# Kernel optimization log

Measured on AMD Instinct MI355X. Metric: run time of the kernel, lower is better.

Reference implementation:

```python
import jax, jax.numpy as jnp
import numpy as np

DISTANCE_WEIGHT = 1.001  # self.distence_weight in the torch module


def setup_inputs() -> dict:
    key = jax.random.key(0)
    k1, k2 = jax.random.split(key)
    B, DIM_IN, DIM_OUT = 1024, 512, 512
    x = jax.random.normal(k1, (B, DIM_IN), dtype=jnp.float32)
    centers = jax.random.normal(k2, (DIM_OUT, DIM_IN), dtype=jnp.float32)
    beta = jnp.ones((DIM_OUT,), dtype=jnp.float32)
    return {"x": x, "centers": centers, "beta": beta}


def reference(x, centers, beta):
    # L1 pairwise distance: [B, dim_out]
    sim = jnp.sum(jnp.abs(x[:, None, :] - centers[None, :, :]), axis=-1)
    # negate, shift by global max * distance_weight, scale by beta
    sim = -sim + jnp.max(sim) * DISTANCE_WEIGHT
    return beta * sim
```

## Files before the change

### kernel.cpp

```cpp
#include <hip/hip_runtime.h>


typedef _Float16 h2 __attribute__((ext_vector_type(2)));
typedef float f4 __attribute__((ext_vector_type(4)));
typedef unsigned int u32x4 __attribute__((ext_vector_type(4)));

#define DIM_K 512
#define DIM_O 512
#define NSPLIT 4
#define KW (DIM_K / NSPLIT)
#define PSTRIDE (1024 * 512)
#define W_DIST 1.001f

__device__ __forceinline__ h2 as_h2(unsigned int u){ h2 r; __builtin_memcpy(&r,&u,4); return r; }
__device__ __forceinline__ unsigned int cvt2(float a, float b){
    auto h = __builtin_amdgcn_cvt_pkrtz(a, b);
    unsigned int r; __builtin_memcpy(&r, &h, 4); return r;
}

__global__ __launch_bounds__(256) void k_sim(const float* __restrict__ X,
                                             const float* __restrict__ C,
                                             float* __restrict__ P)
{
    __shared__ __align__(16) unsigned int xs[64 * 64];
    __shared__ __align__(16) unsigned int cs[64 * 64];
    const int tid = threadIdx.x;
    const int b = blockIdx.x;
    const int ks = b & 3;
    const int ct = (b >> 2) & 7;
    const int rt = b >> 5;
    const int row0 = rt * 64, col0 = ct * 64, kb = ks * KW;

#pragma unroll
    for (int p = 0; p < 4; ++p) {
        const int s = tid + 256 * p;
        const int row = s >> 4, gI = s & 15, gg = gI ^ (row & 7);
        const float* xg = X + (row0 + row) * DIM_K + kb + gg * 8;
        f4 a = *(const f4*)xg; f4 bb = *(const f4*)(xg + 4);
        u32x4 w; w[0]=cvt2(a.x,a.y); w[1]=cvt2(a.z,a.w); w[2]=cvt2(bb.x,bb.y); w[3]=cvt2(bb.z,bb.w);
        *(u32x4*)&xs[row * 64 + gI * 4] = w;
        const float* cg = C + (col0 + row) * DIM_K + kb + gg * 8;
        a = *(const f4*)cg; bb = *(const f4*)(cg + 4);
        u32x4 v; v[0]=cvt2(a.x,a.y); v[1]=cvt2(a.z,a.w); v[2]=cvt2(bb.x,bb.y); v[3]=cvt2(bb.z,bb.w);
        *(u32x4*)&cs[row * 64 + gI * 4] = v;
    }
    __syncthreads();

    const int rb = (tid >> 4) * 4;
    const int tc = tid & 15;
    float acc[4][4] = {};
    const h2 one2 = {(_Float16)1.f, (_Float16)1.f};

#pragma unroll
    for (int g = 0; g < 16; ++g) {
        u32x4 xr[4], cr[4];
#pragma unroll
        for (int i = 0; i < 4; ++i) {
            const int r = rb + i;
            xr[i] = *(const u32x4*)&xs[r * 64 + (g ^ (r & 7)) * 4];
        }
#pragma unroll
        for (int j = 0; j < 4; ++j) {
            const int c = tc + 16 * j;
            cr[j] = *(const u32x4*)&cs[c * 64 + (g ^ (c & 7)) * 4];
        }
#pragma unroll
        for (int k2 = 0; k2 < 4; ++k2) {
#pragma unroll
            for (int i = 0; i < 4; ++i) {
                const h2 a = as_h2(xr[i][k2]);
#pragma unroll
                for (int j = 0; j < 4; ++j) {
                    h2 d = a - as_h2(cr[j][k2]);
                    unsigned int du; __builtin_memcpy(&du, &d, 4);
                    h2 ad = as_h2(du & 0x7fff7fffu);
                    acc[i][j] = __builtin_amdgcn_fdot2(ad, one2, acc[i][j], false);
                }
            }
        }
    }

    float* Pk = P + ks * PSTRIDE;
#pragma unroll
    for (int i = 0; i < 4; ++i) {
        const int row = row0 + rb + i;
#pragma unroll
        for (int j = 0; j < 4; ++j)
            Pk[row * DIM_O + col0 + tc + 16 * j] = acc[i][j];
    }
}

__global__ __launch_bounds__(256) void k_red(const float* __restrict__ P,
                                             float* __restrict__ S,
                                             float* __restrict__ bmax)
{
    const int tid = threadIdx.x;
    const int f = blockIdx.x * 256 + tid;
    const f4* P4 = (const f4*)P;
    const int q = PSTRIDE / 4;
    f4 s = P4[f] + P4[f + q] + P4[f + 2 * q] + P4[f + 3 * q];
    ((f4*)S)[f] = s;
    float m = fmaxf(fmaxf(s.x, s.y), fmaxf(s.z, s.w));
#pragma unroll
    for (int off = 32; off > 0; off >>= 1)
        m = fmaxf(m, __shfl_xor(m, off, 64));
    __shared__ float wm[4];
    if ((tid & 63) == 0) wm[tid >> 6] = m;
    __syncthreads();
    if (tid == 0)
        bmax[blockIdx.x] = fmaxf(fmaxf(wm[0], wm[1]), fmaxf(wm[2], wm[3]));
}

__global__ __launch_bounds__(256) void k_out(float* __restrict__ S,
                                             const float* __restrict__ beta,
                                             const float* __restrict__ bmax)
{
    const int tid = threadIdx.x;
    const int lane = tid & 63;
    float m = 0.f;
#pragma unroll
    for (int i = 0; i < 8; ++i)
        m = fmaxf(m, bmax[lane + 64 * i]);
#pragma unroll
    for (int off = 32; off > 0; off >>= 1)
        m = fmaxf(m, __shfl_xor(m, off, 64));
    const float shift = m * W_DIST;

    const int f = blockIdx.x * 256 + tid;
    f4 s = ((const f4*)S)[f];
    f4 b = ((const f4*)beta)[f & 127];
    f4 r;
    r.x = b.x * (shift - s.x);
    r.y = b.y * (shift - s.y);
    r.z = b.z * (shift - s.z);
    r.w = b.w * (shift - s.w);
    ((f4*)S)[f] = r;
}

extern "C" void kernel_launch(void* const* d_in, const int* in_sizes, int n_in,
                              void* d_out, int out_size, void* d_ws, size_t ws_size,
                              hipStream_t stream) {
    const float* X = (const float*)d_in[0];
    const float* C = (const float*)d_in[1];
    const float* beta = (const float*)d_in[2];
    float* S = (float*)d_out;
    float* P = (float*)d_ws;
    float* bmax = (float*)d_ws + NSPLIT * PSTRIDE;
    k_sim<<<512, 256, 0, stream>>>(X, C, P);
    k_red<<<512, 256, 0, stream>>>(P, S, bmax);
    k_out<<<512, 256, 0, stream>>>(S, beta, bmax);
}
```

Baseline: 79.62 us.

## Split K eight ways with padded LDS rows and occupancy hint

Doubles the K split from four to eight, launching 1024 blocks that each cover 64 K-elements. The XOR-swizzled shared layout is replaced by rows padded to 36 words, and each thread now loads a full 16-float chunk. A minimum-occupancy hint of 4 blocks per CU is added to launch bounds. The aim is more blocks in flight to fill the GPU and hide load latency, but the partial-sum buffer doubles in size, so the reduction kernel reads twice as much data.

Measured after the change: 83.53 us. 1.05x slower.

```diff
diff --git a/kernel.cpp b/kernel.cpp
--- a/kernel.cpp
+++ b/kernel.cpp
@@ -7,8 +7,9 @@
 
 #define DIM_K 512
 #define DIM_O 512
-#define NSPLIT 4
+#define NSPLIT 8
 #define KW (DIM_K / NSPLIT)
+#define LROW 36
 #define PSTRIDE (1024 * 512)
 #define W_DIST 1.001f
 
@@ -18,31 +19,36 @@
     unsigned int r; __builtin_memcpy(&r, &h, 4); return r;
 }
 
-__global__ __launch_bounds__(256) void k_sim(const float* __restrict__ X,
-                                             const float* __restrict__ C,
-                                             float* __restrict__ P)
+__global__ __launch_bounds__(256, 4) void k_sim(const float* __restrict__ X,
+                                                const float* __restrict__ C,
+                                                float* __restrict__ P)
 {
-    __shared__ __align__(16) unsigned int xs[64 * 64];
-    __shared__ __align__(16) unsigned int cs[64 * 64];
+    __shared__ __align__(16) unsigned int xs[64 * LROW];
+    __shared__ __align__(16) unsigned int cs[64 * LROW];
     const int tid = threadIdx.x;
     const int b = blockIdx.x;
-    const int ks = b & 3;
-    const int ct = (b >> 2) & 7;
-    const int rt = b >> 5;
+    const int ks = b & 7;
+    const int ct = (b >> 3) & 7;
+    const int rt = b >> 6;
     const int row0 = rt * 64, col0 = ct * 64, kb = ks * KW;
 
-#pragma unroll
-    for (int p = 0; p < 4; ++p) {
-        const int s = tid + 256 * p;
-        const int row = s >> 4, gI = s & 15, gg = gI ^ (row & 7);
-        const float* xg = X + (row0 + row) * DIM_K + kb + gg * 8;
-        f4 a = *(const f4*)xg; f4 bb = *(const f4*)(xg + 4);
-        u32x4 w; w[0]=cvt2(a.x,a.y); w[1]=cvt2(a.z,a.w); w[2]=cvt2(bb.x,bb.y); w[3]=cvt2(bb.z,bb.w);
-        *(u32x4*)&xs[row * 64 + gI * 4] = w;
-        const float* cg = C + (col0 + row) * DIM_K + kb + gg * 8;
-        a = *(const f4*)cg; bb = *(const f4*)(cg + 4);
-        u32x4 v; v[0]=cvt2(a.x,a.y); v[1]=cvt2(a.z,a.w); v[2]=cvt2(bb.x,bb.y); v[3]=cvt2(bb.z,bb.w);
-        *(u32x4*)&cs[row * 64 + gI * 4] = v;
+    {
+        const int row = tid >> 2, q = tid & 3;
+        const float* xg = X + (row0 + row) * DIM_K + kb + q * 16;
+        f4 a0 = *(const f4*)xg, a1 = *(const f4*)(xg + 4),
+           a2 = *(const f4*)(xg + 8), a3 = *(const f4*)(xg + 12);
+        u32x4 w0, w1;
+        w0[0]=cvt2(a0.x,a0.y); w0[1]=cvt2(a0.z,a0.w); w0[2]=cvt2(a1.x,a1.y); w0[3]=cvt2(a1.z,a1.w);
+        w1[0]=cvt2(a2.x,a2.y); w1[1]=cvt2(a2.z,a2.w); w1[2]=cvt2(a3.x,a3.y); w1[3]=cvt2(a3.z,a3.w);
+        *(u32x4*)&xs[row * LROW + q * 8]     = w0;
+        *(u32x4*)&xs[row * LROW + q * 8 + 4] = w1;
+        const float* cg = C + (col0 + row) * DIM_K + kb + q * 16;
+        a0 = *(const f4*)cg; a1 = *(const f4*)(cg + 4);
+        a2 = *(const f4*)(cg + 8); a3 = *(const f4*)(cg + 12);
+        w0[0]=cvt2(a0.x,a0.y); w0[1]=cvt2(a0.z,a0.w); w0[2]=cvt2(a1.x,a1.y); w0[3]=cvt2(a1.z,a1.w);
+        w1[0]=cvt2(a2.x,a2.y); w1[1]=cvt2(a2.z,a2.w); w1[2]=cvt2(a3.x,a3.y); w1[3]=cvt2(a3.z,a3.w);
+        *(u32x4*)&cs[row * LROW + q * 8]     = w0;
+        *(u32x4*)&cs[row * LROW + q * 8 + 4] = w1;
     }
     __syncthreads();
 
@@ -51,19 +57,26 @@
     float acc[4][4] = {};
     const h2 one2 = {(_Float16)1.f, (_Float16)1.f};
 
+    const unsigned int* xb0 = &xs[(rb + 0) * LROW];
+    const unsigned int* xb1 = &xs[(rb + 1) * LROW];
+    const unsigned int* xb2 = &xs[(rb + 2) * LROW];
+    const unsigned int* xb3 = &xs[(rb + 3) * LROW];
+    const unsigned int* cb0 = &cs[(tc +  0) * LROW];
+    const unsigned int* cb1 = &cs[(tc + 16) * LROW];
+    const unsigned int* cb2 = &cs[(tc + 32) * LROW];
+    const unsigned int* cb3 = &cs[(tc + 48) * LROW];
+
 #pragma unroll
-    for (int g = 0; g < 16; ++g) {
+    for (int g = 0; g < 8; ++g) {
         u32x4 xr[4], cr[4];
-#pragma unroll
-        for (int i = 0; i < 4; ++i) {
-            const int r = rb + i;
-            xr[i] = *(const u32x4*)&xs[r * 64 + (g ^ (r & 7)) * 4];
-        }
-#pragma unroll
-        for (int j = 0; j < 4; ++j) {
-            const int c = tc + 16 * j;
-            cr[j] = *(const u32x4*)&cs[c * 64 + (g ^ (c & 7)) * 4];
-        }
+        xr[0] = *(const u32x4*)(xb0 + g * 4);
+        xr[1] = *(const u32x4*)(xb1 + g * 4);
+        xr[2] = *(const u32x4*)(xb2 + g * 4);
+        xr[3] = *(const u32x4*)(xb3 + g * 4);
+        cr[0] = *(const u32x4*)(cb0 + g * 4);
+        cr[1] = *(const u32x4*)(cb1 + g * 4);
+        cr[2] = *(const u32x4*)(cb2 + g * 4);
+        cr[3] = *(const u32x4*)(cb3 + g * 4);
 #pragma unroll
         for (int k2 = 0; k2 < 4; ++k2) {
 #pragma unroll
@@ -98,7 +111,10 @@
     const int f = blockIdx.x * 256 + tid;
     const f4* P4 = (const f4*)P;
     const int q = PSTRIDE / 4;
-    f4 s = P4[f] + P4[f + q] + P4[f + 2 * q] + P4[f + 3 * q];
+    f4 s = P4[f];
+#pragma unroll
+    for (int p = 1; p < NSPLIT; ++p)
+        s += P4[f + p * q];
     ((f4*)S)[f] = s;
     float m = fmaxf(fmaxf(s.x, s.y), fmaxf(s.z, s.w));
 #pragma unroll
@@ -146,7 +162,7 @@
     float* S = (float*)d_out;
     float* P = (float*)d_ws;
     float* bmax = (float*)d_ws + NSPLIT * PSTRIDE;
-    k_sim<<<512, 256, 0, stream>>>(X, C, P);
+    k_sim<<<1024, 256, 0, stream>>>(X, C, P);
     k_red<<<512, 256, 0, stream>>>(P, S, bmax);
     k_out<<<512, 256, 0, stream>>>(S, beta, bmax);
 }
```
